# Optimization experiments

Measured on AMD Instinct MI355X. Metric: run time of the kernel, lower is better.

## Reference

```python
import jax, jax.numpy as jnp
import numpy as np

IN_DIM = 256
HIDDEN = 256
N_TAPES = 2
DIM = HIDDEN // N_TAPES          # 128
LSTM_H = 8 * N_TAPES             # 16
SEQ = 256
BATCH = 32
TAPELEN = 256


def setup_inputs() -> dict:
    key = jax.random.key(0)
    ks = jax.random.split(key, 10)
    s = 0.05
    inputs = jax.random.normal(ks[0], (SEQ, BATCH, IN_DIM), jnp.float32)
    # LSTM params (torch gate order: i, f, g, o)
    W_ih = s * jax.random.normal(ks[1], (4 * LSTM_H, IN_DIM), jnp.float32)
    W_hh = s * jax.random.normal(ks[2], (4 * LSTM_H, LSTM_H), jnp.float32)
    b_ih = s * jax.random.normal(ks[3], (4 * LSTM_H,), jnp.float32)
    b_hh = s * jax.random.normal(ks[4], (4 * LSTM_H,), jnp.float32)
    # value / out linear layers
    W_val = s * jax.random.normal(ks[5], (HIDDEN, IN_DIM), jnp.float32)
    b_val = s * jax.random.normal(ks[6], (HIDDEN,), jnp.float32)
    W_out = s * jax.random.normal(ks[7], (HIDDEN, HIDDEN), jnp.float32)
    b_out = s * jax.random.normal(ks[8], (HIDDEN,), jnp.float32)
    return {
        'inputs': inputs, 'tapelen': TAPELEN,
        'W_ih': W_ih, 'W_hh': W_hh, 'b_ih': b_ih, 'b_hh': b_hh,
        'W_val': W_val, 'b_val': b_val, 'W_out': W_out, 'b_out': b_out,
    }


def _lstm(inputs, W_ih, W_hh, b_ih, b_hh):
    # inputs: [S, B, in_dim] -> hidden seq [S, B, LSTM_H], torch gate order i,f,g,o
    S, B, _ = inputs.shape
    xg = inputs @ W_ih.T + (b_ih + b_hh)  # precompute input contribution [S,B,4H]

    def step(carry, xt):
        h, c = carry
        g = xt + h @ W_hh.T
        i, f, gg, o = jnp.split(g, 4, axis=-1)
        c = jax.nn.sigmoid(f) * c + jax.nn.sigmoid(i) * jnp.tanh(gg)
        h = jax.nn.sigmoid(o) * jnp.tanh(c)
        return (h, c), h

    h0 = jnp.zeros((B, W_hh.shape[1]), inputs.dtype)
    (_, _), hs = jax.lax.scan(step, (h0, h0), xg)
    return hs


def reference(inputs, tapelen, W_ih, W_hh, b_ih, b_hh, W_val, b_val, W_out, b_out):
    seqlen, bs, _ = inputs.shape
    values = (inputs @ W_val.T + b_val).reshape(seqlen, bs, N_TAPES, DIM)

    actions = _lstm(inputs, W_ih, W_hh, b_ih, b_hh).reshape(seqlen, bs, N_TAPES, 8)
    dirs_r = jax.nn.softmax(actions[..., 0:3], axis=-1)
    dirs_w = jax.nn.softmax(actions[..., 3:6], axis=-1)
    rwprobs = jax.nn.sigmoid(actions[..., 6:8])

    tape0 = jnp.zeros((tapelen, bs, N_TAPES, DIM), inputs.dtype)
    pos0 = jnp.zeros((tapelen, bs, N_TAPES), inputs.dtype).at[0].set(1.0)

    def step(carry, xs):
        tape, rpos, wpos = carry
        v, rd, wd, rw = xs  # v:[B,T,C] rd/wd:[B,T,3] rw:[B,T,2]
        # write: replace value at soft write position, gated by rw[...,1]
        oldval = jnp.einsum('lntc,lnt->ntc', tape, wpos)
        newmem = jnp.einsum('lnt,ntc->lntc', wpos, v - oldval)
        tape = tape + newmem * rw[None, :, :, 1:2]
        # NOTE: faithful to source — write-position shifts roll rpos, not wpos
        next_w = jnp.roll(rpos, 1, axis=0)
        prev_w = jnp.roll(rpos, -1, axis=0)
        wpos = prev_w * wd[None, :, :, 0] + wpos * wd[None, :, :, 1] + next_w * wd[None, :, :, 2]
        # read, gated by rw[...,0]
        read_out = jnp.einsum('lntc,lnt->ntc', tape, rpos * rw[None, :, :, 0])
        next_r = jnp.roll(rpos, 1, axis=0)
        prev_r = jnp.roll(rpos, -1, axis=0)
        rpos = prev_r * rd[None, :, :, 0] + rpos * rd[None, :, :, 1] + next_r * rd[None, :, :, 2]
        return (tape, rpos, wpos), read_out

    (tape, rpos, wpos), reads = jax.lax.scan(
        step, (tape0, pos0, pos0), (values, dirs_r, dirs_w, rwprobs))

    outputs = reads.reshape(seqlen, bs, HIDDEN) @ W_out.T + b_out
    return outputs, tape, (rpos, wpos)
```

## Files before the change

### kernel.cpp

```cpp
#include <hip/hip_runtime.h>

#define SEQ    256
#define BATCH  32
#define NT     2
#define DIM    128
#define LTAPE  256

typedef float f32x4 __attribute__((ext_vector_type(4)));
typedef short s16x8 __attribute__((ext_vector_type(8)));
typedef unsigned int u32;
typedef unsigned short u16;

__device__ __forceinline__ float sigm(float x) { return 1.f / (1.f + __expf(-x)); }
__device__ __forceinline__ float tanh_(float x) { float e = __expf(2.f * x); return 1.f - 2.f / (e + 1.f); }
__device__ __forceinline__ u16 f2bf(float x) {
  u32 u = __builtin_bit_cast(u32, x);
  u32 r = (u + 0x7fffu + ((u >> 16) & 1u)) >> 16;
  return (u16)r;
}
__device__ __forceinline__ float bf2f(u16 b) {
  u32 u = ((u32)b) << 16; return __builtin_bit_cast(float, u);
}

template<bool A_BF16, bool OUT_BF16>
__global__ __launch_bounds__(256) void gemm_mfma(
    const void* __restrict__ Av, const float* __restrict__ W,
    const float* __restrict__ bias, void* __restrict__ Cv, int N) {
  __shared__ u16 As[128 * 40];
  __shared__ u16 Bs[64 * 40];
  const int tid = threadIdx.x;
  const int bm = blockIdx.x * 128, bn = blockIdx.y * 64;
  const int wv = tid >> 6, lane = tid & 63;
  const int wm = wv >> 1, wn = wv & 1;
  const int l15 = lane & 15, l4 = lane >> 4;
  f32x4 acc[4][2] = {};
  const int arow = tid >> 1, ahalf = tid & 1;
  const int brow = (tid & 127) >> 1, bhalf = tid & 1;

  for (int k0 = 0; k0 < 256; k0 += 32) {
    u16 abuf[16];
    if (A_BF16) {
      const u16* A = (const u16*)Av;
      const uint4* p = (const uint4*)(A + (size_t)(bm + arow) * 256 + k0 + ahalf * 16);
      *(uint4*)(abuf) = p[0]; *(uint4*)(abuf + 8) = p[1];
    } else {
      const float* A = (const float*)Av;
      const float* src = A + (size_t)(bm + arow) * 256 + k0 + ahalf * 16;
      float4 x0 = ((const float4*)src)[0], x1 = ((const float4*)src)[1];
      float4 x2 = ((const float4*)src)[2], x3 = ((const float4*)src)[3];
      float xs[16] = {x0.x, x0.y, x0.z, x0.w, x1.x, x1.y, x1.z, x1.w,
                      x2.x, x2.y, x2.z, x2.w, x3.x, x3.y, x3.z, x3.w};
#pragma unroll
      for (int j = 0; j < 16; ++j) abuf[j] = f2bf(xs[j]);
    }
    u16 bbuf[16];
    if (tid < 128) {
      const float* src = W + (size_t)(bn + brow) * 256 + k0 + bhalf * 16;
      float4 x0 = ((const float4*)src)[0], x1 = ((const float4*)src)[1];
      float4 x2 = ((const float4*)src)[2], x3 = ((const float4*)src)[3];
      float xs[16] = {x0.x, x0.y, x0.z, x0.w, x1.x, x1.y, x1.z, x1.w,
                      x2.x, x2.y, x2.z, x2.w, x3.x, x3.y, x3.z, x3.w};
#pragma unroll
      for (int j = 0; j < 16; ++j) bbuf[j] = f2bf(xs[j]);
    }
    __syncthreads();
    *(uint4*)&As[arow * 40 + ahalf * 16] = *(const uint4*)(abuf);
    *(uint4*)&As[arow * 40 + ahalf * 16 + 8] = *(const uint4*)(abuf + 8);
    if (tid < 128) {
      *(uint4*)&Bs[brow * 40 + bhalf * 16] = *(const uint4*)(bbuf);
      *(uint4*)&Bs[brow * 40 + bhalf * 16 + 8] = *(const uint4*)(bbuf + 8);
    }
    __syncthreads();
    s16x8 af[4], bfr[2];
#pragma unroll
    for (int mi = 0; mi < 4; ++mi)
      af[mi] = *(const s16x8*)&As[(wm * 64 + mi * 16 + l15) * 40 + l4 * 8];
#pragma unroll
    for (int ni = 0; ni < 2; ++ni)
      bfr[ni] = *(const s16x8*)&Bs[(wn * 32 + ni * 16 + l15) * 40 + l4 * 8];
#pragma unroll
    for (int mi = 0; mi < 4; ++mi)
#pragma unroll
      for (int ni = 0; ni < 2; ++ni)
        acc[mi][ni] = __builtin_amdgcn_mfma_f32_16x16x32_bf16(af[mi], bfr[ni], acc[mi][ni], 0, 0, 0);
  }
#pragma unroll
  for (int mi = 0; mi < 4; ++mi)
#pragma unroll
    for (int ni = 0; ni < 2; ++ni)
#pragma unroll
      for (int r = 0; r < 4; ++r) {
        int row = bm + wm * 64 + mi * 16 + l4 * 4 + r;
        int col = bn + wn * 32 + ni * 16 + l15;
        float val = acc[mi][ni][r] + bias[col];
        if (OUT_BF16) ((u16*)Cv)[(size_t)row * N + col] = f2bf(val);
        else          ((float*)Cv)[(size_t)row * N + col] = val;
      }
}

__global__ __launch_bounds__(256) void gemm_nt(
    const float* __restrict__ A, const float* __restrict__ W,
    const float* __restrict__ b1, const float* __restrict__ b2,
    float* __restrict__ C, int N) {
  __shared__ float Asm[16][68];
  __shared__ float Bsm[16][68];
  const int tid = threadIdx.x;
  const int bm = blockIdx.x * 64;
  const int bn = blockIdx.y * 64;
  const int lr = tid >> 2;
  const int lc4 = (tid & 3) * 4;
  const int tm = (tid & 15) * 4;
  const int tn = (tid >> 4) * 4;
  float acc[4][4];
#pragma unroll
  for (int i = 0; i < 4; ++i)
#pragma unroll
    for (int j = 0; j < 4; ++j) acc[i][j] = 0.f;
  for (int k0 = 0; k0 < 256; k0 += 16) {
    float4 av = *reinterpret_cast<const float4*>(&A[(bm + lr) * 256 + k0 + lc4]);
    float4 bv = *reinterpret_cast<const float4*>(&W[(bn + lr) * 256 + k0 + lc4]);
    __syncthreads();
    Asm[lc4 + 0][lr] = av.x; Asm[lc4 + 1][lr] = av.y; Asm[lc4 + 2][lr] = av.z; Asm[lc4 + 3][lr] = av.w;
    Bsm[lc4 + 0][lr] = bv.x; Bsm[lc4 + 1][lr] = bv.y; Bsm[lc4 + 2][lr] = bv.z; Bsm[lc4 + 3][lr] = bv.w;
    __syncthreads();
#pragma unroll
    for (int kk = 0; kk < 16; ++kk) {
      float4 a = *reinterpret_cast<const float4*>(&Asm[kk][tm]);
      float4 b = *reinterpret_cast<const float4*>(&Bsm[kk][tn]);
      float a_[4] = {a.x, a.y, a.z, a.w};
      float b_[4] = {b.x, b.y, b.z, b.w};
#pragma unroll
      for (int i = 0; i < 4; ++i)
#pragma unroll
        for (int j = 0; j < 4; ++j) acc[i][j] += a_[i] * b_[j];
    }
  }
#pragma unroll
  for (int i = 0; i < 4; ++i)
#pragma unroll
    for (int j = 0; j < 4; ++j) {
      int n = bn + tn + j;
      float bias = b1[n] + (b2 ? b2[n] : 0.f);
      C[(size_t)(bm + tm + i) * N + n] = acc[i][j] + bias;
    }
}

__global__ __launch_bounds__(64, 1) void lstm_kernel(
    const float* __restrict__ xg,
    const float* __restrict__ W_hh,
    float* __restrict__ hout) {
  const int lane = threadIdx.x;
  const int b = blockIdx.x;
  const int k = lane & 15, q = lane >> 4;
  float w[16];
#pragma unroll
  for (int kk = 0; kk < 16; ++kk) w[kk] = W_hh[lane * 16 + kk];
  float h = 0.f, c = 0.f;
  const float* xb = xg + (size_t)b * 64 + lane;
  float xA = xb[0 * 2048];
  float xB = xb[1 * 2048];
  float xC = xb[2 * 2048];
  float xD = xb[3 * 2048];

#define LSTM_STEP(S, XV)                                                     \
  {                                                                          \
    float hb[16];                                                            \
    _Pragma("unroll") for (int kk = 0; kk < 16; ++kk)                        \
      hb[kk] = __shfl(h, kk, 64);                                            \
    float pa = w[0] * hb[0], pb = w[1] * hb[1];                              \
    float pcc = w[2] * hb[2], pd = w[3] * hb[3];                             \
    _Pragma("unroll") for (int kk = 4; kk < 16; kk += 4) {                   \
      pa += w[kk + 0] * hb[kk + 0];                                         \
      pb += w[kk + 1] * hb[kk + 1];                                         \
      pcc += w[kk + 2] * hb[kk + 2];                                        \
      pd += w[kk + 3] * hb[kk + 3];                                         \
    }                                                                        \
    float g = XV + (pa + pb) + (pcc + pd);                                   \
    float gi = __shfl(g, k, 64);                                             \
    float gf = __shfl(g, 16 + k, 64);                                        \
    float gg = __shfl(g, 32 + k, 64);                                        \
    float go = __shfl(g, 48 + k, 64);                                        \
    c = sigm(gf) * c + sigm(gi) * tanh_(gg);                                 \
    h = sigm(go) * tanh_(c);                                                 \
    if (q == 0) hout[(size_t)((S) * 32 + b) * 16 + k] = h;                   \
  }

  for (int s0 = 0; s0 < SEQ; s0 += 4) {
    int p4 = s0 + 4; if (p4 > 255) p4 = 255;
    int p5 = s0 + 5; if (p5 > 255) p5 = 255;
    int p6 = s0 + 6; if (p6 > 255) p6 = 255;
    int p7 = s0 + 7; if (p7 > 255) p7 = 255;
    float nA = xb[(size_t)p4 * 2048];
    float nB = xb[(size_t)p5 * 2048];
    float nC = xb[(size_t)p6 * 2048];
    float nD = xb[(size_t)p7 * 2048];
    LSTM_STEP(s0 + 0, xA);
    LSTM_STEP(s0 + 1, xB);
    LSTM_STEP(s0 + 2, xC);
    LSTM_STEP(s0 + 3, xD);
    xA = nA; xB = nB; xC = nC; xD = nD;
  }
#undef LSTM_STEP
}

__global__ __launch_bounds__(256) void head_kernel(
    const float* __restrict__ hout,
    float* __restrict__ pc) {
  const int idx = blockIdx.x * 256 + threadIdx.x;
  const int e = idx & 7, s = (idx >> 3) & 255, p = idx >> 11;
  const int b = p >> 1, t = p & 1;
  const float* hp = hout + ((size_t)(s * 32 + b)) * 16 + t * 8;
  float outv;
  if (e < 3) {
    float a0 = hp[0], a1 = hp[1], a2 = hp[2];
    float m = fmaxf(a0, fmaxf(a1, a2));
    float e0 = __expf(a0 - m), e1 = __expf(a1 - m), e2 = __expf(a2 - m);
    float inv = 1.f / (e0 + e1 + e2);
    outv = (e == 0 ? e0 : (e == 1 ? e1 : e2)) * inv;
  } else if (e < 6) {
    float a3 = hp[3], a4 = hp[4], a5 = hp[5];
    float m = fmaxf(a3, fmaxf(a4, a5));
    float e0 = __expf(a3 - m), e1 = __expf(a4 - m), e2 = __expf(a5 - m);
    float inv = 1.f / (e0 + e1 + e2);
    outv = (e == 3 ? e0 : (e == 4 ? e1 : e2)) * inv;
  } else {
    outv = sigm(hp[e]);
  }
  pc[idx] = outv;
}

__global__ __launch_bounds__(64, 1) void pos_kernel(
    const float* __restrict__ pc,
    float* __restrict__ posW, float* __restrict__ posRs,
    float* __restrict__ out_rpos, float* __restrict__ out_wpos) {
  const int p = blockIdx.x, lane = threadIdx.x;
  float r0 = 0, r1 = 0, r2 = 0, r3 = 0, w0 = 0, w1 = 0, w2 = 0, w3 = 0;
  if (lane == 0) { r0 = 1.f; w0 = 1.f; }
  const float* pcb = pc + (size_t)p * 2048;
  float4 c0 = *(const float4*)&pcb[0];
  float4 c1 = *(const float4*)&pcb[4];
  for (int s0 = 0; s0 < SEQ; s0 += 4) {
    float4 pf[8];
#pragma unroll
    for (int u = 0; u < 4; ++u) {
      int sn = s0 + u + 1; if (sn > 255) sn = 255;
      pf[2 * u]     = *(const float4*)&pcb[sn * 8];
      pf[2 * u + 1] = *(const float4*)&pcb[sn * 8 + 4];
    }
#pragma unroll
    for (int u = 0; u < 4; ++u) {
      const int s = s0 + u;
      size_t ob = ((size_t)p * 256 + s) * 256 + lane * 4;
      *(float4*)(posW + ob) = make_float4(w0, w1, w2, w3);
      float rw0 = c1.z;
      *(float4*)(posRs + ob) = make_float4(r0 * rw0, r1 * rw0, r2 * rw0, r3 * rw0);
      const float crd0 = c0.x, crd1 = c0.y, crd2 = c0.z;
      const float cwd0 = c0.w, cwd1 = c1.x, cwd2 = c1.y;
      float rn  = __shfl(r0, (lane + 1) & 63, 64);
      float rpv = __shfl(r3, (lane + 63) & 63, 64);
      float nw0 = r1 * cwd0 + w0 * cwd1 + rpv * cwd2;
      float nr0 = r1 * crd0 + r0 * crd1 + rpv * crd2;
      float nw1 = r2 * cwd0 + w1 * cwd1 + r0 * cwd2;
      float nr1 = r2 * crd0 + r1 * crd1 + r0 * crd2;
      float nw2 = r3 * cwd0 + w2 * cwd1 + r1 * cwd2;
      float nr2 = r3 * crd0 + r2 * crd1 + r1 * crd2;
      float nw3 = rn * cwd0 + w3 * cwd1 + r2 * cwd2;
      float nr3 = rn * crd0 + r3 * crd1 + r2 * crd2;
      r0 = nr0; r1 = nr1; r2 = nr2; r3 = nr3;
      w0 = nw0; w1 = nw1; w2 = nw2; w3 = nw3;
      c0 = pf[2 * u]; c1 = pf[2 * u + 1];
    }
  }
  out_rpos[(size_t)(lane * 4 + 0) * 64 + p] = r0;
  out_rpos[(size_t)(lane * 4 + 1) * 64 + p] = r1;
  out_rpos[(size_t)(lane * 4 + 2) * 64 + p] = r2;
  out_rpos[(size_t)(lane * 4 + 3) * 64 + p] = r3;
  out_wpos[(size_t)(lane * 4 + 0) * 64 + p] = w0;
  out_wpos[(size_t)(lane * 4 + 1) * 64 + p] = w1;
  out_wpos[(size_t)(lane * 4 + 2) * 64 + p] = w2;
  out_wpos[(size_t)(lane * 4 + 3) * 64 + p] = w3;
}

template<bool TRANS_A, bool B_NT, int MODE, int OUTK, int BROW>
__global__ __launch_bounds__(256) void bgemm(
    const float* __restrict__ A, const float* __restrict__ B,
    const float* __restrict__ pc, float* __restrict__ C,
    size_t sA, size_t sB) {
  __shared__ u16 Ah[128 * 40], Al[128 * 40], Bh[64 * 40], Bl[64 * 40];
  const int p = blockIdx.z;
  const int bm = blockIdx.y * 128, bn = blockIdx.x * 64;
  const int tid = threadIdx.x, wv = tid >> 6, lane = tid & 63;
  const int wm = wv >> 1, wn = wv & 1, l15 = lane & 15, l4 = lane >> 4;
  const int b = p >> 1, t = p & 1;

  if (MODE == 1 && bn >= bm + 128) return;
  if (MODE == 2 && bn >= bm + 128) {
#pragma unroll
    for (int mi = 0; mi < 4; ++mi)
#pragma unroll
      for (int ni = 0; ni < 2; ++ni)
#pragma unroll
        for (int r = 0; r < 4; ++r) {
          int row = bm + wm * 64 + mi * 16 + l4 * 4 + r;
          int col = bn + wn * 32 + ni * 16 + l15;
          C[(size_t)p * 65536 + (size_t)row * 256 + col] = 0.f;
        }
    return;
  }

  const float* Ap = A + (size_t)p * sA;
  const float* Bp = B + (size_t)p * sB;
  f32x4 acc[4][2] = {};

  for (int k0 = 0; k0 < 256; k0 += 32) {
    float xa[16];
    if (!TRANS_A) {
      const int m = tid >> 1, kq = (tid & 1) * 16;
      const float* src = Ap + (size_t)(bm + m) * 256 + k0 + kq;
#pragma unroll
      for (int j = 0; j < 4; ++j) *(float4*)(xa + j * 4) = ((const float4*)src)[j];
    } else {
      const int kr = tid >> 3, mq = (tid & 7) * 16;
      const float* src = Ap + (size_t)(k0 + kr) * 256 + bm + mq;
#pragma unroll
      for (int j = 0; j < 4; ++j) *(float4*)(xa + j * 4) = ((const float4*)src)[j];
    }
    u16 ah[16], al[16];
#pragma unroll
    for (int j = 0; j < 16; ++j) {
      u16 hh = f2bf(xa[j]);
      ah[j] = hh; al[j] = f2bf(xa[j] - bf2f(hh));
    }
    float xb[8];
    if (B_NT) {
      const int n = tid >> 2, kq = (tid & 3) * 8;
      const float* src = Bp + (size_t)(bn + n) * 256 + k0 + kq;
      *(float4*)(xb) = ((const float4*)src)[0];
      *(float4*)(xb + 4) = ((const float4*)src)[1];
    } else {
      const int kr = tid >> 3, nq = (tid & 7) * 8;
      const float* src = Bp + (size_t)(k0 + kr) * BROW + bn + nq;
      *(float4*)(xb) = ((const float4*)src)[0];
      *(float4*)(xb + 4) = ((const float4*)src)[1];
    }
    u16 bh[8], bl[8];
#pragma unroll
    for (int j = 0; j < 8; ++j) {
      u16 hh = f2bf(xb[j]);
      bh[j] = hh; bl[j] = f2bf(xb[j] - bf2f(hh));
    }
    __syncthreads();
    if (!TRANS_A) {
      const int m = tid >> 1, kq = (tid & 1) * 16;
      *(uint4*)&Ah[m * 40 + kq]     = *(const uint4*)(ah);
      *(uint4*)&Ah[m * 40 + kq + 8] = *(const uint4*)(ah + 8);
      *(uint4*)&Al[m * 40 + kq]     = *(const uint4*)(al);
      *(uint4*)&Al[m * 40 + kq + 8] = *(const uint4*)(al + 8);
    } else {
      const int kr = tid >> 3, mq = (tid & 7) * 16;
#pragma unroll
      for (int j = 0; j < 16; ++j) {
        Ah[(mq + j) * 40 + kr] = ah[j];
        Al[(mq + j) * 40 + kr] = al[j];
      }
    }
    if (B_NT) {
      const int n = tid >> 2, kq = (tid & 3) * 8;
      *(uint4*)&Bh[n * 40 + kq] = *(const uint4*)(bh);
      *(uint4*)&Bl[n * 40 + kq] = *(const uint4*)(bl);
    } else {
      const int kr = tid >> 3, nq = (tid & 7) * 8;
#pragma unroll
      for (int j = 0; j < 8; ++j) {
        Bh[(nq + j) * 40 + kr] = bh[j];
        Bl[(nq + j) * 40 + kr] = bl[j];
      }
    }
    __syncthreads();
    s16x8 fah[4], fal[4], fbh[2], fbl[2];
#pragma unroll
    for (int mi = 0; mi < 4; ++mi) {
      fah[mi] = *(const s16x8*)&Ah[(wm * 64 + mi * 16 + l15) * 40 + l4 * 8];
      fal[mi] = *(const s16x8*)&Al[(wm * 64 + mi * 16 + l15) * 40 + l4 * 8];
    }
#pragma unroll
    for (int ni = 0; ni < 2; ++ni) {
      fbh[ni] = *(const s16x8*)&Bh[(wn * 32 + ni * 16 + l15) * 40 + l4 * 8];
      fbl[ni] = *(const s16x8*)&Bl[(wn * 32 + ni * 16 + l15) * 40 + l4 * 8];
    }
#pragma unroll
    for (int mi = 0; mi < 4; ++mi)
#pragma unroll
      for (int ni = 0; ni < 2; ++ni) {
        acc[mi][ni] = __builtin_amdgcn_mfma_f32_16x16x32_bf16(fah[mi], fbh[ni], acc[mi][ni], 0, 0, 0);
        acc[mi][ni] = __builtin_amdgcn_mfma_f32_16x16x32_bf16(fah[mi], fbl[ni], acc[mi][ni], 0, 0, 0);
        acc[mi][ni] = __builtin_amdgcn_mfma_f32_16x16x32_bf16(fal[mi], fbh[ni], acc[mi][ni], 0, 0, 0);
      }
  }
#pragma unroll
  for (int mi = 0; mi < 4; ++mi)
#pragma unroll
    for (int ni = 0; ni < 2; ++ni)
#pragma unroll
      for (int r = 0; r < 4; ++r) {
        int row = bm + wm * 64 + mi * 16 + l4 * 4 + r;
        int col = bn + wn * 32 + ni * 16 + l15;
        float v = acc[mi][ni][r];
        if (MODE == 1) v = (col < row) ? v * pc[((size_t)p * 256 + row) * 8 + 7] : 0.f;
        if (MODE == 2) v = (col <= row) ? v : 0.f;
        if (OUTK == 0)      C[(size_t)p * 65536 + (size_t)row * 256 + col] = v;
        else if (OUTK == 1) C[((size_t)(row * 32 + b)) * 256 + t * 128 + col] = v;
        else                C[((size_t)row * 64 + p) * 128 + col] = v;
      }
}

__global__ __launch_bounds__(256) void solve_kernel(
    const float* __restrict__ L,
    const u16* __restrict__ values,
    const float* __restrict__ pc,
    float* __restrict__ delta) {
  const int p = blockIdx.x >> 1, half = blockIdx.x & 1;
  const int b = p >> 1, t = p & 1;
  const int tid = threadIdx.x, w = tid >> 6, lane = tid & 63;
  __shared__ float ds[256][64];
  __shared__ float Ps[32][64];
  __shared__ float Db[32][33];
  const float* Lp = L + (size_t)p * 65536;

  for (int k = 0; k < 8; ++k) {
    const int s0 = k * 32;
    float acc[8];
#pragma unroll
    for (int i = 0; i < 8; ++i) {
      const int s = s0 + w * 8 + i;
      float rv = bf2f(values[((size_t)(s * 32 + b)) * 256 + t * 128 + half * 64 + lane]);
      acc[i] = rv * pc[((size_t)p * 256 + s) * 8 + 7];
    }
    const float* Lr0 = Lp + (size_t)(s0 + w * 8) * 256;
#pragma unroll 4
    for (int j = 0; j < s0; ++j) {
      float dj = ds[j][lane];
#pragma unroll
      for (int i = 0; i < 8; ++i) acc[i] -= Lr0[(size_t)i * 256 + j] * dj;
    }
    {
      const int r = tid >> 3, q0 = (tid & 7) * 4;
      float4 dv = *(const float4*)(Lp + (size_t)(s0 + r) * 256 + s0 + q0);
      Db[r][q0] = dv.x; Db[r][q0 + 1] = dv.y; Db[r][q0 + 2] = dv.z; Db[r][q0 + 3] = dv.w;
    }
#pragma unroll
    for (int i = 0; i < 8; ++i) Ps[w * 8 + i][lane] = acc[i];
    __syncthreads();
    if (w == 0) {
      float d[32];
#pragma unroll
      for (int r = 0; r < 32; ++r) {
        float xa = Ps[r][lane], xb = 0.f;
#pragma unroll
        for (int q = 0; q < 32; ++q) {
          if (q < r) {
            if (q & 1) xb -= Db[r][q] * d[q];
            else       xa -= Db[r][q] * d[q];
          }
        }
        float x = xa + xb;
        d[r] = x;
        ds[s0 + r][lane] = x;
        delta[((size_t)p * 256 + s0 + r) * 128 + half * 64 + lane] = x;
      }
    }
    __syncthreads();
  }
}

extern "C" void kernel_launch(void* const* d_in, const int* in_sizes, int n_in,
                              void* d_out, int out_size, void* d_ws, size_t ws_size,
                              hipStream_t stream) {
  const float* inputs = (const float*)d_in[0];
  const float* W_ih = (const float*)d_in[2];
  const float* W_hh = (const float*)d_in[3];
  const float* b_ih = (const float*)d_in[4];
  const float* b_hh = (const float*)d_in[5];
  const float* W_val = (const float*)d_in[6];
  const float* b_val = (const float*)d_in[7];
  const float* W_out = (const float*)d_in[8];
  const float* b_out = (const float*)d_in[9];

  float* out = (float*)d_out;
  float* out_tape = out + 2097152;
  float* out_rpos = out + 4194304;
  float* out_wpos = out + 4210688;

  char* ws = (char*)d_ws;
  float* posW      = (float*)(ws);
  float* posRs     = (float*)(ws + 16777216);
  float* LHm       = (float*)(ws + 33554432);
  u16*   values_bf = (u16*)  (ws + 50331648);
  float* xg        = (float*)(ws + 54525952);
  float* delta     = (float*)(ws + 54525952);
  float* pcb       = (float*)(ws + 62914560);
  float* hout      = (float*)(ws + 63438848);
  float* reads_f32 = posRs;

  gemm_mfma<false, true><<<dim3(64, 4), 256, 0, stream>>>(inputs, W_val, b_val, values_bf, 256);
  gemm_nt<<<dim3(128, 1), 256, 0, stream>>>(inputs, W_ih, b_ih, b_hh, xg, 64);
  lstm_kernel<<<32, 64, 0, stream>>>(xg, W_hh, hout);
  head_kernel<<<512, 256, 0, stream>>>(hout, pcb);
  pos_kernel<<<64, 64, 0, stream>>>(pcb, posW, posRs, out_rpos, out_wpos);
  bgemm<false, true, 1, 0, 256><<<dim3(4, 2, 64), 256, 0, stream>>>(
      posW, posW, pcb, LHm, 65536, 65536);
  solve_kernel<<<128, 256, 0, stream>>>(LHm, values_bf, pcb, delta);
  bgemm<false, true, 2, 0, 256><<<dim3(4, 2, 64), 256, 0, stream>>>(
      posRs, posW, pcb, LHm, 65536, 65536);
  bgemm<false, false, 0, 1, 128><<<dim3(2, 2, 64), 256, 0, stream>>>(
      LHm, delta, pcb, reads_f32, 65536, 32768);
  bgemm<true, false, 0, 2, 128><<<dim3(2, 2, 64), 256, 0, stream>>>(
      posW, delta, pcb, out_tape, 65536, 32768);
  gemm_mfma<false, false><<<dim3(64, 4), 256, 0, stream>>>(reads_f32, W_out, b_out, out, 256);
}
```

Measured before the change: 441.1 us.

## Precompute diagonal block inverses and run triangular solve on bf16x3 MFMA

Adds an inv_kernel that inverts each 32x32 diagonal block of the unit-lower-triangular matrix and stores the inverse as split hi/lo bf16 in MFMA fragment layout. solve_kernel now does the off-diagonal update and the diagonal-block solve with 16x16x32 bf16 MFMAs, using a three-product hi/lo split to approximate fp32 accuracy, instead of scalar FMA loops where one wave worked alone on the serial diagonal solve. This is meant to remove the scalar FLOP and serialization cost of the blocked forward substitution. In exchange it adds a kernel launch, bf16-split rounding error, and heavy LDS use that allows only one block per CU.

```diff
diff --git a/kernel.cpp b/kernel.cpp
--- a/kernel.cpp
+++ b/kernel.cpp
@@ -414,60 +414,165 @@
       }
 }
 
-__global__ __launch_bounds__(256) void solve_kernel(
+__global__ __launch_bounds__(64) void inv_kernel(
+    const float* __restrict__ L,
+    u16* __restrict__ MgH, u16* __restrict__ MgL) {
+  const int pk = blockIdx.x;
+  const int p = pk >> 3, s0 = (pk & 7) * 32;
+  const int lane = threadIdx.x;
+  __shared__ float Db[32][33];
+  __shared__ float Ms[32][33];
+  const float* Lp = L + (size_t)p * 65536;
+  {
+    const int r = lane >> 1, c0 = (lane & 1) * 16;
+    const float* src = Lp + (size_t)(s0 + r) * 256 + s0 + c0;
+    float4 v0 = ((const float4*)src)[0], v1 = ((const float4*)src)[1];
+    float4 v2 = ((const float4*)src)[2], v3 = ((const float4*)src)[3];
+    *(float4*)&Db[r][c0]      = v0; *(float4*)&Db[r][c0 + 4]  = v1;
+    *(float4*)&Db[r][c0 + 8]  = v2; *(float4*)&Db[r][c0 + 12] = v3;
+  }
+  __syncthreads();
+  if (lane < 32) {
+    const int j = lane;
+    float m[32];
+#pragma unroll
+    for (int r = 0; r < 32; ++r) {
+      float xa = (r == j) ? 1.f : 0.f;
+      float xb = 0.f;
+#pragma unroll
+      for (int q = 0; q < 32; ++q) {
+        if (q < r) {
+          if (q & 1) xb -= Db[r][q] * m[q];
+          else       xa -= Db[r][q] * m[q];
+        }
+      }
+      float x = xa + xb;
+      m[r] = x;
+      Ms[r][j] = x;
+    }
+  }
+  __syncthreads();
+  const int l15 = lane & 15, l4 = lane >> 4;
+#pragma unroll
+  for (int rt = 0; rt < 2; ++rt) {
+    u32 wh[4], wl[4];
+#pragma unroll
+    for (int i2 = 0; i2 < 4; ++i2) {
+      float v0 = Ms[rt * 16 + l15][l4 * 8 + i2 * 2];
+      float v1 = Ms[rt * 16 + l15][l4 * 8 + i2 * 2 + 1];
+      u16 h0 = f2bf(v0), h1 = f2bf(v1);
+      u16 g0 = f2bf(v0 - bf2f(h0)), g1 = f2bf(v1 - bf2f(h1));
+      wh[i2] = (u32)h0 | ((u32)h1 << 16);
+      wl[i2] = (u32)g0 | ((u32)g1 << 16);
+    }
+    size_t off = (((size_t)pk * 2 + rt) * 64 + lane) * 8;
+    *(uint4*)(MgH + off) = make_uint4(wh[0], wh[1], wh[2], wh[3]);
+    *(uint4*)(MgL + off) = make_uint4(wl[0], wl[1], wl[2], wl[3]);
+  }
+}
+
+__global__ __launch_bounds__(256, 1) void solve_kernel(
     const float* __restrict__ L,
     const u16* __restrict__ values,
     const float* __restrict__ pc,
+    const u16* __restrict__ MgH, const u16* __restrict__ MgL,
     float* __restrict__ delta) {
-  const int p = blockIdx.x >> 1, half = blockIdx.x & 1;
+  const int p = blockIdx.x >> 1, hf = blockIdx.x & 1;
   const int b = p >> 1, t = p & 1;
   const int tid = threadIdx.x, w = tid >> 6, lane = tid & 63;
-  __shared__ float ds[256][64];
-  __shared__ float Ps[32][64];
-  __shared__ float Db[32][33];
+  const int l15 = lane & 15, l4 = lane >> 4;
+  const int col = w * 16 + l15;
+  __shared__ u16 dBsH[64][264];
+  __shared__ u16 dBsL[64][264];
+  __shared__ u16 Lh[32][264];
+  __shared__ u16 Ll[32][264];
+  __shared__ u16 accTH[64][40];
+  __shared__ u16 accTL[64][40];
   const float* Lp = L + (size_t)p * 65536;
+  const int srow = tid >> 3, sseg = tid & 7;
 
   for (int k = 0; k < 8; ++k) {
     const int s0 = k * 32;
-    float acc[8];
-#pragma unroll
-    for (int i = 0; i < 8; ++i) {
-      const int s = s0 + w * 8 + i;
-      float rv = bf2f(values[((size_t)(s * 32 + b)) * 256 + t * 128 + half * 64 + lane]);
-      acc[i] = rv * pc[((size_t)p * 256 + s) * 8 + 7];
-    }
-    const float* Lr0 = Lp + (size_t)(s0 + w * 8) * 256;
-#pragma unroll 4
-    for (int j = 0; j < s0; ++j) {
-      float dj = ds[j][lane];
-#pragma unroll
-      for (int i = 0; i < 8; ++i) acc[i] -= Lr0[(size_t)i * 256 + j] * dj;
+    f32x4 acc0 = {}, acc1 = {};
+#pragma unroll
+    for (int r = 0; r < 4; ++r) {
+      int s = s0 + l4 * 4 + r;
+      float rv = bf2f(values[((size_t)(s * 32 + b)) * 256 + t * 128 + hf * 64 + col]);
+      acc0[r] = rv * pc[((size_t)p * 256 + s) * 8 + 7];
+      int s2 = s + 16;
+      float rv2 = bf2f(values[((size_t)(s2 * 32 + b)) * 256 + t * 128 + hf * 64 + col]);
+      acc1[r] = rv2 * pc[((size_t)p * 256 + s2) * 8 + 7];
+    }
+    size_t mo0 = (((size_t)(p * 8 + k) * 2 + 0) * 64 + lane) * 8;
+    size_t mo1 = (((size_t)(p * 8 + k) * 2 + 1) * 64 + lane) * 8;
+    s16x8 mh0 = *(const s16x8*)(MgH + mo0);
+    s16x8 mh1 = *(const s16x8*)(MgH + mo1);
+    s16x8 ml0 = *(const s16x8*)(MgL + mo0);
+    s16x8 ml1 = *(const s16x8*)(MgL + mo1);
+    for (int c4 = sseg; c4 * 4 < s0; c4 += 8) {
+      float4 lv = *(const float4*)(Lp + (size_t)(s0 + srow) * 256 + c4 * 4);
+      float x0 = -lv.x, x1 = -lv.y, x2 = -lv.z, x3 = -lv.w;
+      u16 h0 = f2bf(x0), h1 = f2bf(x1), h2 = f2bf(x2), h3 = f2bf(x3);
+      u16 g0 = f2bf(x0 - bf2f(h0)), g1 = f2bf(x1 - bf2f(h1));
+      u16 g2 = f2bf(x2 - bf2f(h2)), g3 = f2bf(x3 - bf2f(h3));
+      *(uint2*)&Lh[srow][c4 * 4] = make_uint2((u32)h0 | ((u32)h1 << 16), (u32)h2 | ((u32)h3 << 16));
+      *(uint2*)&Ll[srow][c4 * 4] = make_uint2((u32)g0 | ((u32)g1 << 16), (u32)g2 | ((u32)g3 << 16));
+    }
+    __syncthreads();
+    for (int m = 0; m < k; ++m) {
+      s16x8 bh = *(const s16x8*)&dBsH[col][m * 32 + l4 * 8];
+      s16x8 bl = *(const s16x8*)&dBsL[col][m * 32 + l4 * 8];
+      s16x8 a0h = *(const s16x8*)&Lh[l15][m * 32 + l4 * 8];
+      s16x8 a0l = *(const s16x8*)&Ll[l15][m * 32 + l4 * 8];
+      s16x8 a1h = *(const s16x8*)&Lh[16 + l15][m * 32 + l4 * 8];
+      s16x8 a1l = *(const s16x8*)&Ll[16 + l15][m * 32 + l4 * 8];
+      acc0 = __builtin_amdgcn_mfma_f32_16x16x32_bf16(a0h, bh, acc0, 0, 0, 0);
+      acc0 = __builtin_amdgcn_mfma_f32_16x16x32_bf16(a0h, bl, acc0, 0, 0, 0);
+      acc0 = __builtin_amdgcn_mfma_f32_16x16x32_bf16(a0l, bh, acc0, 0, 0, 0);
+      acc1 = __builtin_amdgcn_mfma_f32_16x16x32_bf16(a1h, bh, acc1, 0, 0, 0);
+      acc1 = __builtin_amdgcn_mfma_f32_16x16x32_bf16(a1h, bl, acc1, 0, 0, 0);
+      acc1 = __builtin_amdgcn_mfma_f32_16x16x32_bf16(a1l, bh, acc1, 0, 0, 0);
     }
     {
-      const int r = tid >> 3, q0 = (tid & 7) * 4;
-      float4 dv = *(const float4*)(Lp + (size_t)(s0 + r) * 256 + s0 + q0);
-      Db[r][q0] = dv.x; Db[r][q0 + 1] = dv.y; Db[r][q0 + 2] = dv.z; Db[r][q0 + 3] = dv.w;
-    }
-#pragma unroll
-    for (int i = 0; i < 8; ++i) Ps[w * 8 + i][lane] = acc[i];
-    __syncthreads();
-    if (w == 0) {
-      float d[32];
-#pragma unroll
-      for (int r = 0; r < 32; ++r) {
-        float xa = Ps[r][lane], xb = 0.f;
-#pragma unroll
-        for (int q = 0; q < 32; ++q) {
-          if (q < r) {
-            if (q & 1) xb -= Db[r][q] * d[q];
-            else       xa -= Db[r][q] * d[q];
-          }
-        }
-        float x = xa + xb;
-        d[r] = x;
-        ds[s0 + r][lane] = x;
-        delta[((size_t)p * 256 + s0 + r) * 128 + half * 64 + lane] = x;
-      }
+      u16 th[8], tl[8];
+#pragma unroll
+      for (int r = 0; r < 4; ++r) {
+        u16 h = f2bf(acc0[r]); th[r] = h; tl[r] = f2bf(acc0[r] - bf2f(h));
+        u16 h2 = f2bf(acc1[r]); th[4 + r] = h2; tl[4 + r] = f2bf(acc1[r] - bf2f(h2));
+      }
+      *(uint2*)&accTH[col][l4 * 4]      = make_uint2((u32)th[0] | ((u32)th[1] << 16), (u32)th[2] | ((u32)th[3] << 16));
+      *(uint2*)&accTH[col][16 + l4 * 4] = make_uint2((u32)th[4] | ((u32)th[5] << 16), (u32)th[6] | ((u32)th[7] << 16));
+      *(uint2*)&accTL[col][l4 * 4]      = make_uint2((u32)tl[0] | ((u32)tl[1] << 16), (u32)tl[2] | ((u32)tl[3] << 16));
+      *(uint2*)&accTL[col][16 + l4 * 4] = make_uint2((u32)tl[4] | ((u32)tl[5] << 16), (u32)tl[6] | ((u32)tl[7] << 16));
+    }
+    f32x4 d0 = {}, d1 = {};
+    {
+      s16x8 bh = *(const s16x8*)&accTH[col][l4 * 8];
+      s16x8 bl = *(const s16x8*)&accTL[col][l4 * 8];
+      d0 = __builtin_amdgcn_mfma_f32_16x16x32_bf16(mh0, bh, d0, 0, 0, 0);
+      d0 = __builtin_amdgcn_mfma_f32_16x16x32_bf16(mh0, bl, d0, 0, 0, 0);
+      d0 = __builtin_amdgcn_mfma_f32_16x16x32_bf16(ml0, bh, d0, 0, 0, 0);
+      d1 = __builtin_amdgcn_mfma_f32_16x16x32_bf16(mh1, bh, d1, 0, 0, 0);
+      d1 = __builtin_amdgcn_mfma_f32_16x16x32_bf16(mh1, bl, d1, 0, 0, 0);
+      d1 = __builtin_amdgcn_mfma_f32_16x16x32_bf16(ml1, bh, d1, 0, 0, 0);
+    }
+#pragma unroll
+    for (int r = 0; r < 4; ++r) {
+      int row0 = l4 * 4 + r;
+      delta[((size_t)p * 256 + s0 + row0) * 128 + hf * 64 + col] = d0[r];
+      delta[((size_t)p * 256 + s0 + 16 + row0) * 128 + hf * 64 + col] = d1[r];
+    }
+    {
+      u16 dh[8], dl[8];
+#pragma unroll
+      for (int r = 0; r < 4; ++r) {
+        u16 h = f2bf(d0[r]); dh[r] = h; dl[r] = f2bf(d0[r] - bf2f(h));
+        u16 h2 = f2bf(d1[r]); dh[4 + r] = h2; dl[4 + r] = f2bf(d1[r] - bf2f(h2));
+      }
+      *(uint2*)&dBsH[col][s0 + l4 * 4]      = make_uint2((u32)dh[0] | ((u32)dh[1] << 16), (u32)dh[2] | ((u32)dh[3] << 16));
+      *(uint2*)&dBsH[col][s0 + 16 + l4 * 4] = make_uint2((u32)dh[4] | ((u32)dh[5] << 16), (u32)dh[6] | ((u32)dh[7] << 16));
+      *(uint2*)&dBsL[col][s0 + l4 * 4]      = make_uint2((u32)dl[0] | ((u32)dl[1] << 16), (u32)dl[2] | ((u32)dl[3] << 16));
+      *(uint2*)&dBsL[col][s0 + 16 + l4 * 4] = make_uint2((u32)dl[4] | ((u32)dl[5] << 16), (u32)dl[6] | ((u32)dl[7] << 16));
     }
     __syncthreads();
   }
@@ -500,6 +605,8 @@
   float* delta     = (float*)(ws + 54525952);
   float* pcb       = (float*)(ws + 62914560);
   float* hout      = (float*)(ws + 63438848);
+  u16*   MgH       = (u16*)  (ws + 63963136);
+  u16*   MgL       = (u16*)  (ws + 65011712);
   float* reads_f32 = posRs;
 
   gemm_mfma<false, true><<<dim3(64, 4), 256, 0, stream>>>(inputs, W_val, b_val, values_bf, 256);
@@ -509,7 +616,8 @@
   pos_kernel<<<64, 64, 0, stream>>>(pcb, posW, posRs, out_rpos, out_wpos);
   bgemm<false, true, 1, 0, 256><<<dim3(4, 2, 64), 256, 0, stream>>>(
       posW, posW, pcb, LHm, 65536, 65536);
-  solve_kernel<<<128, 256, 0, stream>>>(LHm, values_bf, pcb, delta);
+  inv_kernel<<<512, 64, 0, stream>>>(LHm, MgH, MgL);
+  solve_kernel<<<128, 256, 0, stream>>>(LHm, values_bf, pcb, MgH, MgL, delta);
   bgemm<false, true, 2, 0, 256><<<dim3(4, 2, 64), 256, 0, stream>>>(
       posRs, posW, pcb, LHm, 65536, 65536);
   bgemm<false, false, 0, 1, 128><<<dim3(2, 2, 64), 256, 0, stream>>>(
```

Result: faster. 380.8 us (-13.7%).
